# Performance work log

Measured on AMD Instinct MI355X. Metric: run time of the kernel, lower is better.

## Reference

```python
import jax, jax.numpy as jnp
import numpy as np

T, H, I, E, K = 8192, 1024, 2048, 8, 2


def setup_inputs() -> dict:
    key = jax.random.key(0)
    ks = jax.random.split(key, 6)
    s_h = 1.0 / np.sqrt(H)
    s_i = 1.0 / np.sqrt(I)
    return {
        "x": jax.random.normal(ks[0], (T, H), dtype=jnp.float32),
        "Wr": jax.random.normal(ks[1], (H, E), dtype=jnp.float32) * s_h,
        "br": jnp.zeros((E,), dtype=jnp.float32),
        "Wg": jax.random.normal(ks[2], (E, H, I), dtype=jnp.float32) * s_h,
        "Wu": jax.random.normal(ks[3], (E, H, I), dtype=jnp.float32) * s_h,
        "Wd": jax.random.normal(ks[4], (E, I, H), dtype=jnp.float32) * s_i,
    }


def reference(x, Wr, br, Wg, Wu, Wd):
    # Router: dense GEMM + top-k + sigmoid gate renormalization
    logits = x @ Wr + br                            # [T, E]
    topk_vals, topk_idx = jax.lax.top_k(logits, K)  # [T, K]
    g = jax.nn.sigmoid(topk_vals)
    g = g / (jnp.sum(g, axis=-1, keepdims=True) + 1e-10)
    # Scatter gates to dense [T, E] combine weights (zero for unselected experts)
    gates = jnp.zeros((x.shape[0], Wr.shape[1]), dtype=x.dtype)
    gates = gates.at[jnp.arange(x.shape[0])[:, None], topk_idx].add(g)
    # SwiGLU expert MLP, computed densely over experts and combined by gates
    h_gate = jnp.einsum("th,ehi->tei", x, Wg)       # [T, E, I]
    h_up = jnp.einsum("th,ehi->tei", x, Wu)
    h = jax.nn.silu(h_gate) * h_up
    h = h * gates[:, :, None]                       # fuse gate combine before down-proj
    out = jnp.einsum("tei,eih->th", h, Wd)          # [T, H]
    return out
```

## Files before the change

### kernel.cpp

```cpp
#include <hip/hip_runtime.h>
#include <hip/hip_bf16.h>
#include <stdint.h>

#define TT 8192
#define HH 1024
#define II 2048
#define EE 8
#define TOPK 2

typedef __bf16 bf16x8 __attribute__((ext_vector_type(8)));
typedef float f32x4 __attribute__((ext_vector_type(4)));
typedef unsigned short us8 __attribute__((ext_vector_type(8)));

__device__ __forceinline__ unsigned short f2bf(float f) {
  union { float f; unsigned int u; } c; c.f = f;
  unsigned int u = c.u;
  u += 0x7FFFu + ((u >> 16) & 1u);
  return (unsigned short)(u >> 16);
}

__device__ __forceinline__ void gload_lds16(const void* g, void* l) {
  __builtin_amdgcn_global_load_lds((const __attribute__((address_space(1))) void*)g,
                                   (__attribute__((address_space(3))) void*)l, 16, 0, 0);
}

struct RouterSm {
  float wrt[8][1024];
  int lcount[8];
  int lbase[8];
  short ent_e[128];
  short ent_slot[128];
  float ent_g[128];
};
struct TransSm {
  float tile[64][65];
};

#define NTRANS (3 * EE * 512)
#define NZERO 512
__global__ __launch_bounds__(256) void k_prep(
    const float* __restrict__ x, const float* __restrict__ Wr,
    const float* __restrict__ br,
    const float* __restrict__ Wg, const float* __restrict__ Wu,
    const float* __restrict__ Wd,
    unsigned short* __restrict__ xb,
    unsigned short* __restrict__ WguT, unsigned short* __restrict__ WdT,
    int* __restrict__ tlist, float* __restrict__ glist,
    int* __restrict__ counts, float* __restrict__ outz) {
  __shared__ __align__(16) char smem[sizeof(RouterSm)];
  const int bid = blockIdx.x;
  const int tid = threadIdx.x;

  if (bid >= 128 + NTRANS) {
    const int zb = bid - 128 - NTRANS;
    float4 z = {0.f, 0.f, 0.f, 0.f};
    float4* dst = reinterpret_cast<float4*>(outz) + (size_t)zb * 4096 + tid;
#pragma unroll
    for (int i = 0; i < 16; ++i) dst[i * 256] = z;
    return;
  }

  if (bid < 128) {
    RouterSm& R = *reinterpret_cast<RouterSm*>(smem);
    for (int i = tid; i < 8192; i += 256) R.wrt[i & 7][i >> 3] = Wr[i];
    if (tid < 8) R.lcount[tid] = 0;
    __syncthreads();
    int w = tid >> 6, l = tid & 63;
    int t0 = bid * 64;
    for (int it = 0; it < 16; ++it) {
      int t = t0 + w * 16 + it;
      const float4* xr = reinterpret_cast<const float4*>(x + (size_t)t * HH);
      float acc[8] = {0.f, 0.f, 0.f, 0.f, 0.f, 0.f, 0.f, 0.f};
#pragma unroll
      for (int j = 0; j < 4; ++j) {
        float4 xv = xr[j * 64 + l];
        int hbase = (j * 64 + l) * 4;
        ushort4 o;
        o.x = f2bf(xv.x); o.y = f2bf(xv.y); o.z = f2bf(xv.z); o.w = f2bf(xv.w);
        *reinterpret_cast<ushort4*>(xb + (size_t)t * HH + hbase) = o;
#pragma unroll
        for (int e = 0; e < 8; ++e) {
          float4 wv = *reinterpret_cast<const float4*>(&R.wrt[e][hbase]);
          acc[e] += xv.x * wv.x + xv.y * wv.y + xv.z * wv.z + xv.w * wv.w;
        }
      }
#pragma unroll
      for (int e = 0; e < 8; ++e)
#pragma unroll
        for (int off = 32; off > 0; off >>= 1) acc[e] += __shfl_xor(acc[e], off, 64);
      if (l == 0) {
        float lg[8];
#pragma unroll
        for (int e = 0; e < 8; ++e) lg[e] = acc[e] + br[e];
        int i0 = 0;
#pragma unroll
        for (int e = 1; e < 8; ++e) if (lg[e] > lg[i0]) i0 = e;
        int i1 = (i0 == 0) ? 1 : 0;
#pragma unroll
        for (int e = 0; e < 8; ++e) if (e != i0 && lg[e] > lg[i1]) i1 = e;
        float g0 = 1.f / (1.f + expf(-lg[i0]));
        float g1 = 1.f / (1.f + expf(-lg[i1]));
        float inv = 1.f / (g0 + g1 + 1e-10f);
        int idx = (w * 16 + it) * 2;
        int s0 = atomicAdd(&R.lcount[i0], 1);
        R.ent_e[idx] = (short)i0; R.ent_slot[idx] = (short)s0; R.ent_g[idx] = g0 * inv;
        int s1 = atomicAdd(&R.lcount[i1], 1);
        R.ent_e[idx + 1] = (short)i1; R.ent_slot[idx + 1] = (short)s1; R.ent_g[idx + 1] = g1 * inv;
      }
    }
    __syncthreads();
    if (tid < 8) R.lbase[tid] = atomicAdd(&counts[tid], R.lcount[tid]);
    __syncthreads();
    if (tid < 128) {
      int e = R.ent_e[tid];
      int slot = R.lbase[e] + R.ent_slot[tid];
      int t = t0 + (tid >> 1);
      tlist[e * TT + slot] = t;
      glist[e * TT + slot] = R.ent_g[tid];
    }
    return;
  }

  TransSm& T = *reinterpret_cast<TransSm*>(smem);
  const int tb = bid - 128;
  const int job = tb / 4096;
  const int rem = tb - job * 4096;
  const int e = rem >> 9;
  const int xt = rem & 511;
  const float* src; int C, r0, c0;
  if (job < 2) {
    src = (job ? Wu : Wg) + (size_t)e * HH * II;
    C = II; c0 = (xt & 31) * 64; r0 = (xt >> 5) * 64;
  } else {
    src = Wd + (size_t)e * II * HH;
    C = HH; c0 = (xt & 15) * 64; r0 = (xt >> 4) * 64;
  }
  const int tx = tid & 15, ty = tid >> 4;
#pragma unroll
  for (int i = 0; i < 4; ++i) {
    int rr = i * 16 + ty;
    float4 v = *reinterpret_cast<const float4*>(&src[(size_t)(r0 + rr) * C + c0 + tx * 4]);
    T.tile[rr][tx * 4 + 0] = v.x; T.tile[rr][tx * 4 + 1] = v.y;
    T.tile[rr][tx * 4 + 2] = v.z; T.tile[rr][tx * 4 + 3] = v.w;
  }
  __syncthreads();
#pragma unroll
  for (int i = 0; i < 2; ++i) {
    int idx = i * 256 + tid;
    int cc = idx >> 3, ch = idx & 7;
    us8 o;
#pragma unroll
    for (int j = 0; j < 8; ++j) o[j] = f2bf(T.tile[ch * 8 + j][cc]);
    if (job < 2) {
      int srow = c0 * 2 + ((cc >> 4) << 5) + job * 16 + (cc & 15);
      *reinterpret_cast<us8*>(&WguT[((size_t)e * 2 * II + srow) * HH + r0 + ch * 8]) = o;
    } else {
      *reinterpret_cast<us8*>(&WdT[((size_t)e * HH + c0 + cc) * II + r0 + ch * 8]) = o;
    }
  }
}

__global__ __launch_bounds__(256, 4) void k_gemm1(
    const unsigned short* __restrict__ xb,
    const unsigned short* __restrict__ WguT,
    const int* __restrict__ tlist, const float* __restrict__ glist,
    const int* __restrict__ counts,
    unsigned short* __restrict__ hbuf) {
  __shared__ unsigned short lsA[128 * 64];
  __shared__ unsigned short lsB[128 * 64];
  __shared__ int s_tok[128];
  __shared__ float s_gate[128];

  const int e = blockIdx.z;
  int n_e = 0, obase = 0;
#pragma unroll
  for (int q = 0; q < EE; ++q) {
    int c = counts[q];
    if (q < e) obase += c;
    if (q == e) n_e = c;
  }
  const int row0 = blockIdx.y * 128;
  if (row0 >= n_e) return;
  const int n0 = blockIdx.x * 128;
  const int tid = threadIdx.x;

  if (tid < 128) {
    int r = row0 + tid;
    int tok = 0; float gt = 0.f;
    if (r < n_e) { tok = tlist[e * TT + r]; gt = glist[e * TT + r]; }
    s_tok[tid] = tok; s_gate[tid] = gt;
  }
  __syncthreads();

  const int scol = (tid & 7) ^ ((tid >> 3) & 7);
  const unsigned short* srcA[4];
  const unsigned short* srcB[4];
#pragma unroll
  for (int i = 0; i < 4; ++i) {
    int row = i * 32 + (tid >> 3);
    srcA[i] = xb + (size_t)s_tok[row] * HH + scol * 8;
    srcB[i] = WguT + ((size_t)e * 2 * II + n0 + row) * HH + scol * 8;
  }

  f32x4 zero = {0.f, 0.f, 0.f, 0.f};
  f32x4 acc[4][4];
#pragma unroll
  for (int m = 0; m < 4; ++m)
#pragma unroll
    for (int n = 0; n < 4; ++n) acc[m][n] = zero;

  const int l = tid & 63;
  const int w = tid >> 6;
  const int wr = (w >> 1) * 64;
  const int wc = (w & 1) * 64;
  const int lrow = l & 15;
  const int lk = l >> 4;
  const int swz = (l & 7) << 4;
  const int aoff0 = (wr + lrow) * 128 + lk * 16;
  const int boff0 = (wc + lrow) * 128 + lk * 16;
  const char* lcA = (const char*)lsA;
  const char* lcB = (const char*)lsB;

  for (int kt = 0; kt < HH / 64; ++kt) {
#pragma unroll
    for (int i = 0; i < 4; ++i) {
      gload_lds16(srcA[i] + kt * 64, (char*)lsA + i * 4096 + tid * 16);
      gload_lds16(srcB[i] + kt * 64, (char*)lsB + i * 4096 + tid * 16);
    }
    __syncthreads();
#pragma unroll
    for (int kk = 0; kk < 2; ++kk) {
      bf16x8 af[4], bf[4];
#pragma unroll
      for (int m = 0; m < 4; ++m)
        af[m] = *(const bf16x8*)(lcA + ((aoff0 + m * 2048 + kk * 64) ^ swz));
#pragma unroll
      for (int n = 0; n < 4; ++n)
        bf[n] = *(const bf16x8*)(lcB + ((boff0 + n * 2048 + kk * 64) ^ swz));
#pragma unroll
      for (int m = 0; m < 4; ++m)
#pragma unroll
        for (int n = 0; n < 4; ++n)
          acc[m][n] = __builtin_amdgcn_mfma_f32_16x16x32_bf16(af[m], bf[n], acc[m][n], 0, 0, 0);
    }
    __syncthreads();
  }

#pragma unroll
  for (int m = 0; m < 4; ++m)
#pragma unroll
    for (int n = 0; n < 4; n += 2)
#pragma unroll
      for (int r = 0; r < 4; ++r) {
        int rl = wr + m * 16 + lk * 4 + r;
        if (row0 + rl < n_e) {
          float gv = acc[m][n][r];
          float uv = acc[m][n + 1][r];
          float val = gv / (1.f + __expf(-gv)) * uv * s_gate[rl];
          int L = (n0 >> 1) + (wc >> 1) + (n >> 1) * 16 + lrow;
          hbuf[(size_t)(obase + row0 + rl) * II + L] = f2bf(val);
        }
      }
}

__global__ __launch_bounds__(256, 4) void k_gemm2(
    const unsigned short* __restrict__ hbuf,
    const unsigned short* __restrict__ WdT,
    const int* __restrict__ tlist,
    const int* __restrict__ counts,
    float* __restrict__ out) {
  __shared__ unsigned short lsA[128 * 64];
  __shared__ unsigned short lsB[128 * 64];
  __shared__ int s_tok[128];

  const int e = blockIdx.z;
  int n_e = 0, obase = 0;
#pragma unroll
  for (int q = 0; q < EE; ++q) {
    int c = counts[q];
    if (q < e) obase += c;
    if (q == e) n_e = c;
  }
  const int row0 = blockIdx.y * 128;
  if (row0 >= n_e) return;
  const int n0 = blockIdx.x * 128;
  const int tid = threadIdx.x;

  if (tid < 128) {
    int r = row0 + tid;
    s_tok[tid] = (r < n_e) ? tlist[e * TT + r] : 0;
  }
  __syncthreads();

  const int scol = (tid & 7) ^ ((tid >> 3) & 7);
  const unsigned short* srcA[4];
  const unsigned short* srcB[4];
#pragma unroll
  for (int i = 0; i < 4; ++i) {
    int row = i * 32 + (tid >> 3);
    int ar = obase + row0 + row;
    if (ar > TT * TOPK - 1) ar = TT * TOPK - 1;
    srcA[i] = hbuf + (size_t)ar * II + scol * 8;
    srcB[i] = WdT + ((size_t)e * HH + n0 + row) * II + scol * 8;
  }

  f32x4 zero = {0.f, 0.f, 0.f, 0.f};
  f32x4 acc[4][4];
#pragma unroll
  for (int m = 0; m < 4; ++m)
#pragma unroll
    for (int n = 0; n < 4; ++n) acc[m][n] = zero;

  const int l = tid & 63;
  const int w = tid >> 6;
  const int wr = (w >> 1) * 64;
  const int wc = (w & 1) * 64;
  const int lrow = l & 15;
  const int lk = l >> 4;
  const int swz = (l & 7) << 4;
  const int aoff0 = (wr + lrow) * 128 + lk * 16;
  const int boff0 = (wc + lrow) * 128 + lk * 16;
  const char* lcA = (const char*)lsA;
  const char* lcB = (const char*)lsB;

  for (int kt = 0; kt < II / 64; ++kt) {
#pragma unroll
    for (int i = 0; i < 4; ++i) {
      gload_lds16(srcA[i] + kt * 64, (char*)lsA + i * 4096 + tid * 16);
      gload_lds16(srcB[i] + kt * 64, (char*)lsB + i * 4096 + tid * 16);
    }
    __syncthreads();
#pragma unroll
    for (int kk = 0; kk < 2; ++kk) {
      bf16x8 af[4], bf[4];
#pragma unroll
      for (int m = 0; m < 4; ++m)
        af[m] = *(const bf16x8*)(lcA + ((aoff0 + m * 2048 + kk * 64) ^ swz));
#pragma unroll
      for (int n = 0; n < 4; ++n)
        bf[n] = *(const bf16x8*)(lcB + ((boff0 + n * 2048 + kk * 64) ^ swz));
#pragma unroll
      for (int m = 0; m < 4; ++m)
#pragma unroll
        for (int n = 0; n < 4; ++n)
          acc[m][n] = __builtin_amdgcn_mfma_f32_16x16x32_bf16(af[m], bf[n], acc[m][n], 0, 0, 0);
    }
    __syncthreads();
  }

#pragma unroll
  for (int m = 0; m < 4; ++m)
#pragma unroll
    for (int n = 0; n < 4; ++n)
#pragma unroll
      for (int r = 0; r < 4; ++r) {
        int rl = wr + m * 16 + lk * 4 + r;
        if (row0 + rl < n_e) {
          int t = s_tok[rl];
          unsafeAtomicAdd(&out[(size_t)t * HH + n0 + wc + n * 16 + lrow], acc[m][n][r]);
        }
      }
}

extern "C" void kernel_launch(void* const* d_in, const int* in_sizes, int n_in,
                              void* d_out, int out_size, void* d_ws, size_t ws_size,
                              hipStream_t stream) {
  const float* x  = (const float*)d_in[0];
  const float* Wr = (const float*)d_in[1];
  const float* br = (const float*)d_in[2];
  const float* Wg = (const float*)d_in[3];
  const float* Wu = (const float*)d_in[4];
  const float* Wd = (const float*)d_in[5];
  float* out = (float*)d_out;

  char* ws = (char*)d_ws;
  size_t off = 0;
  auto alloc = [&](size_t bytes) {
    char* p = ws + off;
    off += (bytes + 255) & ~(size_t)255;
    return p;
  };
  unsigned short* xb   = (unsigned short*)alloc((size_t)TT * HH * 2);
  unsigned short* WguT = (unsigned short*)alloc((size_t)EE * 2 * II * HH * 2);
  unsigned short* WdT  = (unsigned short*)alloc((size_t)EE * HH * II * 2);
  unsigned short* hbuf = (unsigned short*)alloc((size_t)TT * TOPK * II * 2);
  int*   tlist  = (int*)alloc((size_t)EE * TT * 4);
  float* glist  = (float*)alloc((size_t)EE * TT * 4);
  int*   counts = (int*)alloc(128);

  hipMemsetAsync(counts, 0, 128, stream);

  k_prep<<<128 + NTRANS + NZERO, 256, 0, stream>>>(x, Wr, br, Wg, Wu, Wd,
                                                   xb, WguT, WdT, tlist, glist,
                                                   counts, out);

  dim3 g1(2 * II / 128, TT / 128, EE);
  k_gemm1<<<g1, 256, 0, stream>>>(xb, WguT, tlist, glist, counts, hbuf);
  dim3 g2(HH / 128, TT / 128, EE);
  k_gemm2<<<g2, 256, 0, stream>>>(hbuf, WdT, tlist, counts, out);

  (void)in_sizes; (void)n_in; (void)out_size; (void)ws_size;
}
```

Measured before the change: 346.0 us.

## Pre-swizzle gate/up weights into MFMA fragment order and load B directly to registers

The prep kernel now writes the combined gate/up weights in a fragment-major layout that matches the MFMA B-operand register order for each 128-column by 64-k tile. In gemm1, each wave loads its B fragments straight from global memory into registers with contiguous 16-byte per-lane loads, which removes the B shared-memory buffer and its LDS reads. This halves LDS traffic and footprint in gemm1. In exchange, B loads are no longer shared between the two waves that use the same columns, so global and L2 traffic for the weights doubles, and load latency is exposed inside the loop with no prefetch.

Result: slower. 371.9 us (+7.5%).

```diff
diff --git a/kernel.cpp b/kernel.cpp
--- a/kernel.cpp
+++ b/kernel.cpp
@@ -44,7 +44,7 @@
     const float* __restrict__ Wg, const float* __restrict__ Wu,
     const float* __restrict__ Wd,
     unsigned short* __restrict__ xb,
-    unsigned short* __restrict__ WguT, unsigned short* __restrict__ WdT,
+    unsigned short* __restrict__ WguF, unsigned short* __restrict__ WdT,
     int* __restrict__ tlist, float* __restrict__ glist,
     int* __restrict__ counts, float* __restrict__ outz) {
   __shared__ __align__(16) char smem[sizeof(RouterSm)];
@@ -152,8 +152,11 @@
 #pragma unroll
     for (int j = 0; j < 8; ++j) o[j] = f2bf(T.tile[ch * 8 + j][cc]);
     if (job < 2) {
-      int srow = c0 * 2 + ((cc >> 4) << 5) + job * 16 + (cc & 15);
-      *reinterpret_cast<us8*>(&WguT[((size_t)e * 2 * II + srow) * HH + r0 + ch * 8]) = o;
+      int s = c0 * 2 + ((cc >> 4) << 5) + job * 16 + (cc & 15);
+      size_t off = (((size_t)(e * 32 + (s >> 7)) * 16 + (r0 >> 6)) << 13)
+                 + ((size_t)(((s >> 4) & 7) * 2 + ((ch >> 2) & 1)) << 9)
+                 + ((size_t)((ch & 3) * 16 + (s & 15)) << 3);
+      *reinterpret_cast<us8*>(&WguF[off]) = o;
     } else {
       *reinterpret_cast<us8*>(&WdT[((size_t)e * HH + c0 + cc) * II + r0 + ch * 8]) = o;
     }
@@ -162,12 +165,11 @@
 
 __global__ __launch_bounds__(256, 4) void k_gemm1(
     const unsigned short* __restrict__ xb,
-    const unsigned short* __restrict__ WguT,
+    const unsigned short* __restrict__ WguF,
     const int* __restrict__ tlist, const float* __restrict__ glist,
     const int* __restrict__ counts,
     unsigned short* __restrict__ hbuf) {
   __shared__ unsigned short lsA[128 * 64];
-  __shared__ unsigned short lsB[128 * 64];
   __shared__ int s_tok[128];
   __shared__ float s_gate[128];
 
@@ -194,12 +196,120 @@
 
   const int scol = (tid & 7) ^ ((tid >> 3) & 7);
   const unsigned short* srcA[4];
-  const unsigned short* srcB[4];
 #pragma unroll
   for (int i = 0; i < 4; ++i) {
     int row = i * 32 + (tid >> 3);
     srcA[i] = xb + (size_t)s_tok[row] * HH + scol * 8;
-    srcB[i] = WguT + ((size_t)e * 2 * II + n0 + row) * HH + scol * 8;
+  }
+
+  f32x4 zero = {0.f, 0.f, 0.f, 0.f};
+  f32x4 acc[4][4];
+#pragma unroll
+  for (int m = 0; m < 4; ++m)
+#pragma unroll
+    for (int n = 0; n < 4; ++n) acc[m][n] = zero;
+
+  const int l = tid & 63;
+  const int w = tid >> 6;
+  const int wr = (w >> 1) * 64;
+  const int wc = (w & 1) * 64;
+  const int lrow = l & 15;
+  const int lk = l >> 4;
+  const int swz = (l & 7) << 4;
+  const int aoff0 = (wr + lrow) * 128 + lk * 16;
+  const char* lcA = (const char*)lsA;
+  const int g0 = wc >> 4;
+  const unsigned short* bblk = WguF + ((size_t)(e * 32 + (n0 >> 7)) << 17);
+
+  for (int kt = 0; kt < HH / 64; ++kt) {
+#pragma unroll
+    for (int i = 0; i < 4; ++i)
+      gload_lds16(srcA[i] + kt * 64, (char*)lsA + i * 4096 + tid * 16);
+    __syncthreads();
+
+    const unsigned short* bp = bblk + ((size_t)kt << 13);
+    bf16x8 b0[4], b1[4];
+#pragma unroll
+    for (int n = 0; n < 4; ++n) {
+      b0[n] = *(const bf16x8*)(bp + (((g0 + n) * 2 + 0) << 9) + l * 8);
+      b1[n] = *(const bf16x8*)(bp + (((g0 + n) * 2 + 1) << 9) + l * 8);
+    }
+    bf16x8 af[4];
+#pragma unroll
+    for (int m = 0; m < 4; ++m)
+      af[m] = *(const bf16x8*)(lcA + ((aoff0 + m * 2048) ^ swz));
+#pragma unroll
+    for (int m = 0; m < 4; ++m)
+#pragma unroll
+      for (int n = 0; n < 4; ++n)
+        acc[m][n] = __builtin_amdgcn_mfma_f32_16x16x32_bf16(af[m], b0[n], acc[m][n], 0, 0, 0);
+#pragma unroll
+    for (int m = 0; m < 4; ++m)
+      af[m] = *(const bf16x8*)(lcA + ((aoff0 + m * 2048 + 64) ^ swz));
+#pragma unroll
+    for (int m = 0; m < 4; ++m)
+#pragma unroll
+      for (int n = 0; n < 4; ++n)
+        acc[m][n] = __builtin_amdgcn_mfma_f32_16x16x32_bf16(af[m], b1[n], acc[m][n], 0, 0, 0);
+    __syncthreads();
+  }
+
+#pragma unroll
+  for (int m = 0; m < 4; ++m)
+#pragma unroll
+    for (int n = 0; n < 4; n += 2)
+#pragma unroll
+      for (int r = 0; r < 4; ++r) {
+        int rl = wr + m * 16 + lk * 4 + r;
+        if (row0 + rl < n_e) {
+          float gv = acc[m][n][r];
+          float uv = acc[m][n + 1][r];
+          float val = gv / (1.f + __expf(-gv)) * uv * s_gate[rl];
+          int L = (n0 >> 1) + (wc >> 1) + (n >> 1) * 16 + lrow;
+          hbuf[(size_t)(obase + row0 + rl) * II + L] = f2bf(val);
+        }
+      }
+}
+
+__global__ __launch_bounds__(256, 4) void k_gemm2(
+    const unsigned short* __restrict__ hbuf,
+    const unsigned short* __restrict__ WdT,
+    const int* __restrict__ tlist,
+    const int* __restrict__ counts,
+    float* __restrict__ out) {
+  __shared__ unsigned short lsA[128 * 64];
+  __shared__ unsigned short lsB[128 * 64];
+  __shared__ int s_tok[128];
+
+  const int e = blockIdx.z;
+  int n_e = 0, obase = 0;
+#pragma unroll
+  for (int q = 0; q < EE; ++q) {
+    int c = counts[q];
+    if (q < e) obase += c;
+    if (q == e) n_e = c;
+  }
+  const int row0 = blockIdx.y * 128;
+  if (row0 >= n_e) return;
+  const int n0 = blockIdx.x * 128;
+  const int tid = threadIdx.x;
+
+  if (tid < 128) {
+    int r = row0 + tid;
+    s_tok[tid] = (r < n_e) ? tlist[e * TT + r] : 0;
+  }
+  __syncthreads();
+
+  const int scol = (tid & 7) ^ ((tid >> 3) & 7);
+  const unsigned short* srcA[4];
+  const unsigned short* srcB[4];
+#pragma unroll
+  for (int i = 0; i < 4; ++i) {
+    int row = i * 32 + (tid >> 3);
+    int ar = obase + row0 + row;
+    if (ar > TT * TOPK - 1) ar = TT * TOPK - 1;
+    srcA[i] = hbuf + (size_t)ar * II + scol * 8;
+    srcB[i] = WdT + ((size_t)e * HH + n0 + row) * II + scol * 8;
   }
 
   f32x4 zero = {0.f, 0.f, 0.f, 0.f};
@@ -221,108 +331,6 @@
   const char* lcA = (const char*)lsA;
   const char* lcB = (const char*)lsB;
 
-  for (int kt = 0; kt < HH / 64; ++kt) {
-#pragma unroll
-    for (int i = 0; i < 4; ++i) {
-      gload_lds16(srcA[i] + kt * 64, (char*)lsA + i * 4096 + tid * 16);
-      gload_lds16(srcB[i] + kt * 64, (char*)lsB + i * 4096 + tid * 16);
-    }
-    __syncthreads();
-#pragma unroll
-    for (int kk = 0; kk < 2; ++kk) {
-      bf16x8 af[4], bf[4];
-#pragma unroll
-      for (int m = 0; m < 4; ++m)
-        af[m] = *(const bf16x8*)(lcA + ((aoff0 + m * 2048 + kk * 64) ^ swz));
-#pragma unroll
-      for (int n = 0; n < 4; ++n)
-        bf[n] = *(const bf16x8*)(lcB + ((boff0 + n * 2048 + kk * 64) ^ swz));
-#pragma unroll
-      for (int m = 0; m < 4; ++m)
-#pragma unroll
-        for (int n = 0; n < 4; ++n)
-          acc[m][n] = __builtin_amdgcn_mfma_f32_16x16x32_bf16(af[m], bf[n], acc[m][n], 0, 0, 0);
-    }
-    __syncthreads();
-  }
-
-#pragma unroll
-  for (int m = 0; m < 4; ++m)
-#pragma unroll
-    for (int n = 0; n < 4; n += 2)
-#pragma unroll
-      for (int r = 0; r < 4; ++r) {
-        int rl = wr + m * 16 + lk * 4 + r;
-        if (row0 + rl < n_e) {
-          float gv = acc[m][n][r];
-          float uv = acc[m][n + 1][r];
-          float val = gv / (1.f + __expf(-gv)) * uv * s_gate[rl];
-          int L = (n0 >> 1) + (wc >> 1) + (n >> 1) * 16 + lrow;
-          hbuf[(size_t)(obase + row0 + rl) * II + L] = f2bf(val);
-        }
-      }
-}
-
-__global__ __launch_bounds__(256, 4) void k_gemm2(
-    const unsigned short* __restrict__ hbuf,
-    const unsigned short* __restrict__ WdT,
-    const int* __restrict__ tlist,
-    const int* __restrict__ counts,
-    float* __restrict__ out) {
-  __shared__ unsigned short lsA[128 * 64];
-  __shared__ unsigned short lsB[128 * 64];
-  __shared__ int s_tok[128];
-
-  const int e = blockIdx.z;
-  int n_e = 0, obase = 0;
-#pragma unroll
-  for (int q = 0; q < EE; ++q) {
-    int c = counts[q];
-    if (q < e) obase += c;
-    if (q == e) n_e = c;
-  }
-  const int row0 = blockIdx.y * 128;
-  if (row0 >= n_e) return;
-  const int n0 = blockIdx.x * 128;
-  const int tid = threadIdx.x;
-
-  if (tid < 128) {
-    int r = row0 + tid;
-    s_tok[tid] = (r < n_e) ? tlist[e * TT + r] : 0;
-  }
-  __syncthreads();
-
-  const int scol = (tid & 7) ^ ((tid >> 3) & 7);
-  const unsigned short* srcA[4];
-  const unsigned short* srcB[4];
-#pragma unroll
-  for (int i = 0; i < 4; ++i) {
-    int row = i * 32 + (tid >> 3);
-    int ar = obase + row0 + row;
-    if (ar > TT * TOPK - 1) ar = TT * TOPK - 1;
-    srcA[i] = hbuf + (size_t)ar * II + scol * 8;
-    srcB[i] = WdT + ((size_t)e * HH + n0 + row) * II + scol * 8;
-  }
-
-  f32x4 zero = {0.f, 0.f, 0.f, 0.f};
-  f32x4 acc[4][4];
-#pragma unroll
-  for (int m = 0; m < 4; ++m)
-#pragma unroll
-    for (int n = 0; n < 4; ++n) acc[m][n] = zero;
-
-  const int l = tid & 63;
-  const int w = tid >> 6;
-  const int wr = (w >> 1) * 64;
-  const int wc = (w & 1) * 64;
-  const int lrow = l & 15;
-  const int lk = l >> 4;
-  const int swz = (l & 7) << 4;
-  const int aoff0 = (wr + lrow) * 128 + lk * 16;
-  const int boff0 = (wc + lrow) * 128 + lk * 16;
-  const char* lcA = (const char*)lsA;
-  const char* lcB = (const char*)lsB;
-
   for (int kt = 0; kt < II / 64; ++kt) {
 #pragma unroll
     for (int i = 0; i < 4; ++i) {
@@ -381,7 +389,7 @@
     return p;
   };
   unsigned short* xb   = (unsigned short*)alloc((size_t)TT * HH * 2);
-  unsigned short* WguT = (unsigned short*)alloc((size_t)EE * 2 * II * HH * 2);
+  unsigned short* WguF = (unsigned short*)alloc((size_t)EE * 2 * II * HH * 2);
   unsigned short* WdT  = (unsigned short*)alloc((size_t)EE * HH * II * 2);
   unsigned short* hbuf = (unsigned short*)alloc((size_t)TT * TOPK * II * 2);
   int*   tlist  = (int*)alloc((size_t)EE * TT * 4);
@@ -391,11 +399,11 @@
   hipMemsetAsync(counts, 0, 128, stream);
 
   k_prep<<<128 + NTRANS + NZERO, 256, 0, stream>>>(x, Wr, br, Wg, Wu, Wd,
-                                                   xb, WguT, WdT, tlist, glist,
+                                                   xb, WguF, WdT, tlist, glist,
                                                    counts, out);
 
   dim3 g1(2 * II / 128, TT / 128, EE);
-  k_gemm1<<<g1, 256, 0, stream>>>(xb, WguT, tlist, glist, counts, hbuf);
+  k_gemm1<<<g1, 256, 0, stream>>>(xb, WguF, tlist, glist, counts, hbuf);
   dim3 g2(HH / 128, TT / 128, EE);
   k_gemm2<<<g2, 256, 0, stream>>>(hbuf, WdT, tlist, counts, out);
 
```
